# Optimization experiments

Measured on AMD Instinct MI355X. Metric: run time of the kernel, lower is better.

## Reference

```python
import jax, jax.numpy as jnp
import numpy as np

PERIOD = 24
TREND_WINDOW = 24
HALF = TREND_WINDOW // 2          # 12
DROP = (TREND_WINDOW - 1) // 2    # 11 rows dropped off the batch axis (as in original)


def setup_inputs() -> dict:
    key = jax.random.key(0)
    x = jax.random.normal(key, (4096, 2048), dtype=jnp.float32)
    return {"x": x}


def _trend(x):
    # Centered moving average with boundary-clipped (variable-size) windows,
    # vectorized via an exclusive cumulative sum.  x: (B, T)
    B, T = x.shape
    cs = jnp.concatenate([jnp.zeros((B, 1), x.dtype), jnp.cumsum(x, axis=1)], axis=1)  # (B, T+1)
    i = jnp.arange(T)
    start = jnp.clip(i - HALF, 0, T)           # max(0, i - half_window)
    end = jnp.clip(i + HALF + 1, 0, T)         # min(T, i + half_window + 1)
    sums = cs[:, end] - cs[:, start]           # (B, T)
    counts = (end - start).astype(x.dtype)     # (T,)
    return sums / counts


def _seasonal(x):
    # Phase-wise mean: seasonal[b, t] = mean_{t' : t' % PERIOD == t % PERIOD} x[b, t']
    B, T = x.shape
    phase = jnp.arange(T) % PERIOD                                    # (T,)
    sums = jax.ops.segment_sum(x.T, phase, num_segments=PERIOD)      # (P, B)
    counts = jax.ops.segment_sum(jnp.ones((T,), x.dtype), phase, num_segments=PERIOD)  # (P,)
    means = sums / counts[:, None]                                    # (P, B)
    return means[phase].T                                             # (B, T)


def reference(x):
    trend = _trend(x)
    detrended = x - trend                 # additive method
    seasonal = _seasonal(detrended)
    residual = x - trend - seasonal
    out = jnp.stack([trend, seasonal, residual], axis=2)  # (B, T, 3)
    # drop_na: original slices along the batch axis
    return out[DROP:, :, :]
```

## Files before the change

### kernel.cpp

```cpp
#include <hip/hip_runtime.h>

#define TT 2048
#define BB 4096
#define DROP_ROWS 11
#define NOUT (BB - DROP_ROWS)
#define PERIOD 24
#define BLOCK 256
#define HALF 12
#define ROWS 4

typedef float nfloat4 __attribute__((ext_vector_type(4)));

#define BARRIER() asm volatile("s_waitcnt lgkmcnt(0)\n\ts_barrier" ::: "memory")

__global__ __launch_bounds__(BLOCK) void seasonal_decomp_kernel(
    const float* __restrict__ x, float* __restrict__ out) {
  __shared__ float buf[6144];
  __shared__ float pp2[3][264];
  __shared__ float wt0[4], wt1[4];
  __shared__ float pmean[PERIOD];
  float* const cs = buf;
  float* const sout = buf;

  const int tid = threadIdx.x;
  const int lane = tid & 63;
  const int wave = tid >> 6;
  const int rbase = blockIdx.x * ROWS;

  const int q0 = (512 * wave + lane) % 24;
  int mA, mB, mC;
  if (q0 < 8)       { mA = 0; mB = 2; mC = 1; }
  else if (q0 < 16) { mA = 1; mB = 0; mC = 2; }
  else              { mA = 2; mB = 1; mC = 0; }

  float4 v0, v1;
  if (rbase < NOUT) {
    const float4* rx = (const float4*)(x + (size_t)(rbase + DROP_ROWS) * TT);
    v0 = rx[tid];
    v1 = rx[tid + 256];
  }

  for (int r = 0; r < ROWS; ++r) {
    const int orow_i = rbase + r;
    const bool active = (orow_i < NOUT);

    float s0 = 0.f, s1 = 0.f, i0 = 0.f, i1 = 0.f;
    if (active) {
      s0 = v0.x + v0.y + v0.z + v0.w;
      s1 = v1.x + v1.y + v1.z + v1.w;
      i0 = s0; i1 = s1;
      #pragma unroll
      for (int off = 1; off < 64; off <<= 1) {
        float t0 = __shfl_up(i0, off, 64);
        float t1 = __shfl_up(i1, off, 64);
        if (lane >= off) { i0 += t0; i1 += t1; }
      }
      if (lane == 63) { wt0[wave] = i0; wt1[wave] = i1; }
    }
    BARRIER();

    if (active) {
      float W0 = 0.f, W1 = 0.f, H = 0.f;
      #pragma unroll
      for (int w = 0; w < 4; ++w) {
        float a = wt0[w], b = wt1[w];
        H += a;
        if (w < wave) { W0 += a; W1 += b; }
      }
      const float P0 = W0 + (i0 - s0);
      const float P1 = H + W1 + (i1 - s1);
      float4 c0, c1;
      c0.x = P0; c0.y = P0 + v0.x; c0.z = c0.y + v0.y; c0.w = c0.z + v0.z;
      c1.x = P1; c1.y = P1 + v1.x; c1.z = c1.y + v1.y; c1.w = c1.z + v1.z;
      ((float4*)cs)[tid] = c0;
      ((float4*)cs)[tid + 256] = c1;
      if (tid == 255) cs[TT] = P1 + s1;
    }

    if (r + 1 < ROWS && rbase + r + 1 < NOUT) {
      const float4* rx =
          (const float4*)(x + (size_t)(rbase + r + 1 + DROP_ROWS) * TT);
      v0 = rx[tid];
      v1 = rx[tid + 256];
    }
    BARRIER();

    float tr[8], sdr[8];
    if (active) {
      float A = 0.f, B = 0.f, C2 = 0.f;
      #pragma unroll
      for (int j = 0; j < 8; ++j) {
        const int t = 512 * wave + 64 * j + lane;
        const float xt = cs[t + 1] - cs[t];
        float trv;
        if (t >= HALF && t < TT - HALF - 1) {
          trv = (cs[t + HALF + 1] - cs[t - HALF]) * (1.0f / 25.0f);
        } else {
          const int a = (t - HALF < 0) ? 0 : t - HALF;
          const int e = (t + HALF + 1 > TT) ? TT : t + HALF + 1;
          trv = (cs[e] - cs[a]) / (float)(e - a);
        }
        tr[j] = trv;
        sdr[j] = xt - trv;
        if (j % 3 == 0) A += sdr[j];
        else if (j % 3 == 1) B += sdr[j];
        else C2 += sdr[j];
      }
      pp2[mA][tid] = A;
      pp2[mB][tid] = B;
      pp2[mC][tid] = C2;
    }
    BARRIER();

    if (active && tid < PERIOD) {
      const int c = tid & 7, m = tid >> 3;
      float s = 0.f;
      #pragma unroll
      for (int k = 0; k < 32; ++k) s += pp2[m][8 * k + c];
      pmean[tid] = s * ((tid < 8) ? (1.0f / 86.f) : (1.0f / 85.f));
    }
    BARRIER();

    if (active) {
      float* const mysout = sout + 1536 * wave;
      int p = q0;
      #pragma unroll
      for (int j = 0; j < 8; ++j) {
        const int t64 = 64 * j + lane;
        const float pm = pmean[p];
        p += 16; if (p >= PERIOD) p -= PERIOD;
        mysout[3 * t64]     = tr[j];
        mysout[3 * t64 + 1] = pm;
        mysout[3 * t64 + 2] = sdr[j] - pm;
      }
      const nfloat4* so4 = (const nfloat4*)mysout;
      nfloat4* orow = (nfloat4*)(out + (size_t)orow_i * (TT * 3));
      #pragma unroll
      for (int j = 0; j < 6; ++j) {
        nfloat4 v = so4[64 * j + lane];
        __builtin_nontemporal_store(v, &orow[384 * wave + 64 * j + lane]);
      }
    }
  }
}

extern "C" void kernel_launch(void* const* d_in, const int* in_sizes, int n_in,
                              void* d_out, int out_size, void* d_ws, size_t ws_size,
                              hipStream_t stream) {
  const float* x = (const float*)d_in[0];
  float* out = (float*)d_out;
  const int grid = (NOUT + ROWS - 1) / ROWS;
  seasonal_decomp_kernel<<<grid, BLOCK, 0, stream>>>(x, out);
}
```

Baseline: 26.88 us.

## Double block size to 512 threads with one float4 per thread per row

Widens the block from 256 to 512 threads (8 waves), so each thread handles one float4 of the row instead of two. The scan, trend, phase-sum partition and output store indexing are rebuilt around 8 waves. The goal is more waves per row, giving more latency hiding and parallelism. In exchange there are more wave totals in the cross-wave prefix, a longer 64-step pmean reduction, and barriers over larger blocks.

```diff
diff --git a/kernel.cpp b/kernel.cpp
--- a/kernel.cpp
+++ b/kernel.cpp
@@ -5,7 +5,8 @@
 #define DROP_ROWS 11
 #define NOUT (BB - DROP_ROWS)
 #define PERIOD 24
-#define BLOCK 256
+#define BLOCK 512
+#define NWAVES 8
 #define HALF 12
 #define ROWS 4
 
@@ -16,8 +17,8 @@
 __global__ __launch_bounds__(BLOCK) void seasonal_decomp_kernel(
     const float* __restrict__ x, float* __restrict__ out) {
   __shared__ float buf[6144];
-  __shared__ float pp2[3][264];
-  __shared__ float wt0[4], wt1[4];
+  __shared__ float pp2[3][520];
+  __shared__ float wt[NWAVES];
   __shared__ float pmean[PERIOD];
   float* const cs = buf;
   float* const sout = buf;
@@ -27,73 +28,63 @@
   const int wave = tid >> 6;
   const int rbase = blockIdx.x * ROWS;
 
-  const int q0 = (512 * wave + lane) % 24;
+  const int q0 = (256 * wave + lane) % 24;
   int mA, mB, mC;
   if (q0 < 8)       { mA = 0; mB = 2; mC = 1; }
   else if (q0 < 16) { mA = 1; mB = 0; mC = 2; }
   else              { mA = 2; mB = 1; mC = 0; }
 
-  float4 v0, v1;
+  float4 v0;
   if (rbase < NOUT) {
     const float4* rx = (const float4*)(x + (size_t)(rbase + DROP_ROWS) * TT);
     v0 = rx[tid];
-    v1 = rx[tid + 256];
   }
 
   for (int r = 0; r < ROWS; ++r) {
     const int orow_i = rbase + r;
     const bool active = (orow_i < NOUT);
 
-    float s0 = 0.f, s1 = 0.f, i0 = 0.f, i1 = 0.f;
+    float s = 0.f, i = 0.f;
     if (active) {
-      s0 = v0.x + v0.y + v0.z + v0.w;
-      s1 = v1.x + v1.y + v1.z + v1.w;
-      i0 = s0; i1 = s1;
+      s = v0.x + v0.y + v0.z + v0.w;
+      i = s;
       #pragma unroll
       for (int off = 1; off < 64; off <<= 1) {
-        float t0 = __shfl_up(i0, off, 64);
-        float t1 = __shfl_up(i1, off, 64);
-        if (lane >= off) { i0 += t0; i1 += t1; }
+        float t = __shfl_up(i, off, 64);
+        if (lane >= off) i += t;
       }
-      if (lane == 63) { wt0[wave] = i0; wt1[wave] = i1; }
+      if (lane == 63) wt[wave] = i;
     }
     BARRIER();
 
     if (active) {
-      float W0 = 0.f, W1 = 0.f, H = 0.f;
+      float W = 0.f;
       #pragma unroll
-      for (int w = 0; w < 4; ++w) {
-        float a = wt0[w], b = wt1[w];
-        H += a;
-        if (w < wave) { W0 += a; W1 += b; }
-      }
-      const float P0 = W0 + (i0 - s0);
-      const float P1 = H + W1 + (i1 - s1);
-      float4 c0, c1;
-      c0.x = P0; c0.y = P0 + v0.x; c0.z = c0.y + v0.y; c0.w = c0.z + v0.z;
-      c1.x = P1; c1.y = P1 + v1.x; c1.z = c1.y + v1.y; c1.w = c1.z + v1.z;
-      ((float4*)cs)[tid] = c0;
-      ((float4*)cs)[tid + 256] = c1;
-      if (tid == 255) cs[TT] = P1 + s1;
+      for (int w = 0; w < NWAVES; ++w)
+        if (w < wave) W += wt[w];
+      const float P = W + (i - s);
+      float4 c;
+      c.x = P; c.y = P + v0.x; c.z = c.y + v0.y; c.w = c.z + v0.z;
+      ((float4*)cs)[tid] = c;
+      if (tid == BLOCK - 1) cs[TT] = P + s;
     }
 
     if (r + 1 < ROWS && rbase + r + 1 < NOUT) {
       const float4* rx =
           (const float4*)(x + (size_t)(rbase + r + 1 + DROP_ROWS) * TT);
       v0 = rx[tid];
-      v1 = rx[tid + 256];
     }
     BARRIER();
 
-    float tr[8], sdr[8];
+    float tr[4], sdr[4];
     if (active) {
       float A = 0.f, B = 0.f, C2 = 0.f;
       #pragma unroll
-      for (int j = 0; j < 8; ++j) {
-        const int t = 512 * wave + 64 * j + lane;
+      for (int j = 0; j < 4; ++j) {
+        const int t = 256 * wave + 64 * j + lane;
         const float xt = cs[t + 1] - cs[t];
         float trv;
-        if (t >= HALF && t < TT - HALF - 1) {
+        if (t >= HALF && t < TT - HALF) {
           trv = (cs[t + HALF + 1] - cs[t - HALF]) * (1.0f / 25.0f);
         } else {
           const int a = (t - HALF < 0) ? 0 : t - HALF;
@@ -102,8 +93,8 @@
         }
         tr[j] = trv;
         sdr[j] = xt - trv;
-        if (j % 3 == 0) A += sdr[j];
-        else if (j % 3 == 1) B += sdr[j];
+        if (j == 0 || j == 3) A += sdr[j];
+        else if (j == 1) B += sdr[j];
         else C2 += sdr[j];
       }
       pp2[mA][tid] = A;
@@ -114,18 +105,18 @@
 
     if (active && tid < PERIOD) {
       const int c = tid & 7, m = tid >> 3;
-      float s = 0.f;
+      float sum = 0.f;
       #pragma unroll
-      for (int k = 0; k < 32; ++k) s += pp2[m][8 * k + c];
-      pmean[tid] = s * ((tid < 8) ? (1.0f / 86.f) : (1.0f / 85.f));
+      for (int k = 0; k < 64; ++k) sum += pp2[m][8 * k + c];
+      pmean[tid] = sum * ((tid < 8) ? (1.0f / 86.f) : (1.0f / 85.f));
     }
     BARRIER();
 
     if (active) {
-      float* const mysout = sout + 1536 * wave;
+      float* const mysout = sout + 768 * wave;
       int p = q0;
       #pragma unroll
-      for (int j = 0; j < 8; ++j) {
+      for (int j = 0; j < 4; ++j) {
         const int t64 = 64 * j + lane;
         const float pm = pmean[p];
         p += 16; if (p >= PERIOD) p -= PERIOD;
@@ -136,9 +127,9 @@
       const nfloat4* so4 = (const nfloat4*)mysout;
       nfloat4* orow = (nfloat4*)(out + (size_t)orow_i * (TT * 3));
       #pragma unroll
-      for (int j = 0; j < 6; ++j) {
+      for (int j = 0; j < 3; ++j) {
         nfloat4 v = so4[64 * j + lane];
-        __builtin_nontemporal_store(v, &orow[384 * wave + 64 * j + lane]);
+        __builtin_nontemporal_store(v, &orow[192 * wave + 64 * j + lane]);
       }
     }
   }
```

New measurement: 26.97 us. Within noise of the previous version (+0.3%).
